# Performance work log

Hardware: AMD Instinct MI355X
Metric: run time of the kernel (lower is better)

The kernel has to match this reference:

```python
import jax, jax.numpy as jnp
import numpy as np

GRID_SIZE = 5
SPLINE_ORDER = 3
GRID_LO, GRID_HI = -3.0, 3.0
B, IN_DIM, UNITS, SUB_DIM, NSUB = 4096, 512, 1024, 512, 3


def make_grid(in_features):
    h = (GRID_HI - GRID_LO) / GRID_SIZE
    g = jnp.arange(-SPLINE_ORDER, GRID_SIZE + SPLINE_ORDER + 1, dtype=jnp.float32) * h + GRID_LO
    return jnp.broadcast_to(g, (in_features, g.shape[0]))  # (in, 12)


def b_splines(x, grid):
    # x: (..., in), grid: (in, G) -> (..., in, grid_size + spline_order)
    x = x[..., None]
    bases = ((x >= grid[:, :-1]) & (x < grid[:, 1:])).astype(x.dtype)
    for k in range(1, SPLINE_ORDER + 1):
        left = (x - grid[:, :-(k + 1)]) / (grid[:, k:-1] - grid[:, :-(k + 1)])
        right = (grid[:, k + 1:] - x) / (grid[:, k + 1:] - grid[:, 1:-k])
        bases = left * bases[..., :-1] + right * bases[..., 1:]
    return bases


def setup_inputs() -> dict:
    key = jax.random.key(0)
    ks = jax.random.split(key, 16)
    sw = lambda k, shape, scale: jax.random.normal(k, shape, dtype=jnp.float32) * scale
    inp = {
        'x': sw(ks[0], (B, IN_DIM), 1.0),
        'h0': sw(ks[1], (B, UNITS), 0.1),
        'c0': sw(ks[2], (B, UNITS), 0.1),
        'sub_states': sw(ks[3], (NSUB, B, SUB_DIM), 0.1),
        'kernel': sw(ks[4], (IN_DIM, UNITS * 3), 1.0 / np.sqrt(IN_DIM)),
        'recurrent_kernel': sw(ks[5], (UNITS, UNITS * 3), 1.0 / np.sqrt(UNITS)),
        'bias': jnp.zeros((UNITS * 3,), jnp.float32).at[UNITS:2 * UNITS].set(1.0),
        'sub_kernel_inputs': sw(ks[6], (NSUB, IN_DIM, SUB_DIM), 1.0 / np.sqrt(IN_DIM)),
        'sub_kernel_states': sw(ks[7], (NSUB, SUB_DIM, SUB_DIM), 1.0 / np.sqrt(SUB_DIM)),
        'sub_recurrent_kernel': sw(ks[8], (NSUB, SUB_DIM * 2), 0.5),
        'base_weight': sw(ks[9], (NSUB, SUB_DIM, SUB_DIM), 1.0 / np.sqrt(SUB_DIM)),
        'spline_weight': sw(ks[10], (NSUB, SUB_DIM, SUB_DIM, GRID_SIZE + SPLINE_ORDER), 0.02),
        'spline_scaler': sw(ks[11], (NSUB, SUB_DIM, SUB_DIM), 1.0),
        'aggregated_weight': sw(ks[12], (NSUB * SUB_DIM, UNITS), 1.0 / np.sqrt(NSUB * SUB_DIM)),
        'aggregated_bias': jnp.zeros((UNITS,), jnp.float32),
    }
    return inp


def reference(x, h0, c0, sub_states, kernel, recurrent_kernel, bias,
              sub_kernel_inputs, sub_kernel_states, sub_recurrent_kernel,
              base_weight, spline_weight, spline_scaler,
              aggregated_weight, aggregated_bias):
    grid = make_grid(SUB_DIM)

    # LSTM-style gates: gates = sigmoid(x@W + h@U + b)
    z = x @ kernel + h0 @ recurrent_kernel + bias
    g = jax.nn.sigmoid(z)
    i, f, c_gate = jnp.split(g, 3, axis=-1)
    c_new = f * c0 + i * jnp.tanh(c_gate)

    # Sub-layer inputs: agg[k] = x @ Wx[k] + sub_state[k] @ Wh[k]  -> (k, b, sub_in)
    agg = (jnp.einsum('bi,kis->kbs', x, sub_kernel_inputs)
           + jnp.einsum('kbo,kos->kbs', sub_states, sub_kernel_states))

    # KANLinear: base branch + spline branch (stacked over k sub-layers)
    base_out = jnp.einsum('kbs,kos->kbo', jax.nn.silu(agg), base_weight)
    bases = b_splines(agg, grid)                         # (k, b, sub_in, 8)
    scaled_sw = spline_weight * spline_scaler[..., None]  # (k, out, in, 8)
    spline_out = jnp.einsum('kbic,koic->kbo', bases, scaled_sw)
    sub_out = base_out + spline_out                       # (k, b, sub_out)

    # Recurrent sub-state update
    rk_h = sub_recurrent_kernel[:, None, :SUB_DIM]
    rk_x = sub_recurrent_kernel[:, None, SUB_DIM:]
    new_sub_states = rk_h * sub_out + rk_x * sub_states

    # Output gate from aggregated sub-layer outputs
    agg_flat = jnp.transpose(sub_out, (1, 0, 2)).reshape(x.shape[0], NSUB * SUB_DIM)
    o = jax.nn.sigmoid(agg_flat @ aggregated_weight + aggregated_bias)
    h_new = o * jnp.tanh(c_new)
    return h_new, c_new, new_sub_states
```

## Files before the change

### kernel.cpp

```cpp
#include <hip/hip_runtime.h>

#define B_DIM   4096
#define INF     512
#define UNITS_  1024
#define SUBD    512
#define NSUB_   3
#define NBAS    8
#define G3K     (SUBD * NBAS)

typedef __attribute__((ext_vector_type(8))) short bf16x8_t;
typedef __attribute__((ext_vector_type(4))) float f32x4_t;
typedef unsigned short u16;

__device__ __forceinline__ u16 f2bf(float f) {
    union { float f; unsigned int u; } v; v.f = f;
    unsigned int r = v.u + 0x7fffu + ((v.u >> 16) & 1u);
    return (u16)(r >> 16);
}
__device__ __forceinline__ float bf2f(u16 h) {
    union { unsigned int u; float f; } v; v.u = ((unsigned int)h) << 16;
    return v.f;
}
__device__ __forceinline__ float sigm(float x) { return 1.0f / (1.0f + __expf(-x)); }
__device__ __forceinline__ float tanh_(float x) {
    float e = __expf(2.0f * x);
    return 1.0f - 2.0f / (e + 1.0f);
}

__device__ __forceinline__ void gload_lds16(const void* g, void* l) {
    __builtin_amdgcn_global_load_lds(
        (const __attribute__((address_space(1))) unsigned int*)g,
        (__attribute__((address_space(3))) unsigned int*)l, 16, 0, 0);
}

__global__ void k_f32_to_bf16(const float* __restrict__ in, u16* __restrict__ out, int n4) {
    int i = blockIdx.x * blockDim.x + threadIdx.x;
    if (i >= n4) return;
    float4 v = ((const float4*)in)[i];
    ushort4 r; r.x = f2bf(v.x); r.y = f2bf(v.y); r.z = f2bf(v.z); r.w = f2bf(v.w);
    ((ushort4*)out)[i] = r;
}

__global__ void k_ssw(const float* __restrict__ sw, const float* __restrict__ sc,
                      u16* __restrict__ out, int n4) {
    int i = blockIdx.x * blockDim.x + threadIdx.x;
    if (i >= n4) return;
    float4 v = ((const float4*)sw)[i];
    float s = sc[i >> 1];
    ushort4 r; r.x = f2bf(v.x * s); r.y = f2bf(v.y * s); r.z = f2bf(v.z * s); r.w = f2bf(v.w * s);
    ((ushort4*)out)[i] = r;
}

__global__ void k_tconv(const float* __restrict__ in, u16* __restrict__ out,
                        int R, int C, size_t inStride, size_t outStride) {
    in  += (size_t)blockIdx.z * inStride;
    out += (size_t)blockIdx.z * outStride;
    __shared__ float tile[32][33];
    int c0 = blockIdx.x * 32, r0 = blockIdx.y * 32;
    int tx = threadIdx.x, ty = threadIdx.y;
#pragma unroll
    for (int j = 0; j < 4; ++j)
        tile[ty + j * 8][tx] = in[(size_t)(r0 + ty + j * 8) * C + c0 + tx];
    __syncthreads();
#pragma unroll
    for (int j = 0; j < 4; ++j)
        out[(size_t)(c0 + ty + j * 8) * R + r0 + tx] = f2bf(tile[tx][ty + j * 8]);
}

__global__ void k_cnew(const u16* __restrict__ gbuf, const float* __restrict__ c0,
                       float* __restrict__ c_out, int n4) {
    int i = blockIdx.x * blockDim.x + threadIdx.x;
    if (i >= n4) return;
    int u4 = i * 4;
    int b = u4 >> 10, u = u4 & 1023;
    const u16* gr = gbuf + (size_t)b * 3072 + u;
    ushort4 gi = *(const ushort4*)gr;
    ushort4 gf = *(const ushort4*)(gr + 1024);
    ushort4 gc = *(const ushort4*)(gr + 2048);
    float4 c0v = ((const float4*)c0)[i];
    float4 r;
    r.x = bf2f(gf.x) * c0v.x + bf2f(gi.x) * tanh_(bf2f(gc.x));
    r.y = bf2f(gf.y) * c0v.y + bf2f(gi.y) * tanh_(bf2f(gc.y));
    r.z = bf2f(gf.z) * c0v.z + bf2f(gi.z) * tanh_(bf2f(gc.z));
    r.w = bf2f(gf.w) * c0v.w + bf2f(gi.w) * tanh_(bf2f(gc.w));
    ((float4*)c_out)[i] = r;
}

__global__ void k_bases(const float* __restrict__ agg, u16* __restrict__ bases,
                        u16* __restrict__ silu, int n) {
    for (int i = blockIdx.x * blockDim.x + threadIdx.x; i < n; i += gridDim.x * blockDim.x) {
        float x = agg[i];
        silu[i] = f2bf(x * sigm(x));
        float b[11];
#pragma unroll
        for (int j = 0; j < 11; ++j) {
            float tj  = 1.2f * (float)(j - 3) - 3.0f;
            float tj1 = 1.2f * (float)(j - 2) - 3.0f;
            b[j] = (x >= tj && x < tj1) ? 1.0f : 0.0f;
        }
#pragma unroll
        for (int k = 1; k <= 3; ++k) {
            float inv = 1.0f / (1.2f * (float)k);
#pragma unroll
            for (int j = 0; j < 11; ++j) {
                if (j > 10 - k) break;
                float tj   = 1.2f * (float)(j - 3) - 3.0f;
                float tjk1 = 1.2f * (float)(j + k - 2) - 3.0f;
                b[j] = (x - tj) * inv * b[j] + (tjk1 - x) * inv * b[j + 1];
            }
        }
        bf16x8_t v;
#pragma unroll
        for (int j = 0; j < 8; ++j) v[j] = (short)f2bf(b[j]);
        *(bf16x8_t*)(bases + (size_t)i * 8) = v;
    }
}

struct Seg { const u16* A; const u16* B; int ldA; int ldB; int nkt; };

template<int NS, int BN>
__device__ __forceinline__ void gemm_core(const Seg (&segs)[NS], int rowBase, int colBase,
                                          u16* ldsA, u16* ldsB, f32x4_t (&acc)[4][BN / 32]) {
    constexpr int NACC = BN / 32;
    constexpr int NBC  = BN / 8;
    constexpr int PER  = (16 + NBC) / 4;
    const int t = threadIdx.x;
    const int lane = t & 63, wave = t >> 6;
    const int wR = (wave >> 1) * 64, wC = (wave & 1) * (BN / 2);
    const int l15 = lane & 15, lk = (lane >> 4) * 8;
    const int sr = lane >> 3;
    const int scol = (lane & 7) * 8;
#pragma unroll
    for (int s = 0; s < NS; ++s) {
        const u16* Ag = segs[s].A + (size_t)rowBase * segs[s].ldA;
        const u16* Bg = segs[s].B + (size_t)colBase * segs[s].ldB;
        const int ldA = segs[s].ldA, ldB = segs[s].ldB, nkt = segs[s].nkt;
        for (int kt = 0; kt < nkt; ++kt) {
            __syncthreads();
#pragma unroll
            for (int i = 0; i < PER; ++i) {
                int ci = wave * PER + i;
                if (ci < 16) {
                    int r = ci * 8 + sr;
                    gload_lds16(Ag + (size_t)r * ldA + kt * 64 + scol, ldsA + ci * 512);
                } else {
                    int cb = ci - 16;
                    int r = cb * 8 + sr;
                    gload_lds16(Bg + (size_t)r * ldB + kt * 64 + scol, ldsB + cb * 512);
                }
            }
            __syncthreads();
#pragma unroll
            for (int kk = 0; kk < 2; ++kk) {
                bf16x8_t a[4], b[NACC];
#pragma unroll
                for (int m = 0; m < 4; ++m)
                    a[m] = *(const bf16x8_t*)(ldsA + (wR + m * 16 + l15) * 64 + kk * 32 + lk);
#pragma unroll
                for (int n = 0; n < NACC; ++n)
                    b[n] = *(const bf16x8_t*)(ldsB + (wC + n * 16 + l15) * 64 + kk * 32 + lk);
#pragma unroll
                for (int m = 0; m < 4; ++m)
#pragma unroll
                    for (int n = 0; n < NACC; ++n)
                        acc[m][n] = __builtin_amdgcn_mfma_f32_16x16x32_bf16(a[m], b[n], acc[m][n], 0, 0, 0);
            }
        }
    }
}

template<int NCOL, int NROW, int NWG, bool SWZ>
__device__ __forceinline__ void decode_wg(int o, int& col, int& row, int& kz) {
    int wg = o;
    if (SWZ) {
        constexpr int q = NWG / 8, r = NWG % 8;
        int xcd = o & 7, idx = o >> 3;
        wg = (xcd < r ? xcd * (q + 1) : r * (q + 1) + (xcd - r) * q) + idx;
    }
    col = wg % NCOL; int tmp = wg / NCOL; row = tmp % NROW; kz = tmp / NROW;
}

#define GEMM_PRE(BN, NCOL, NROW, NWG, SWZ)                                 \
    __shared__ u16 ldsA[128 * 64];                                         \
    __shared__ u16 ldsB[BN * 64];                                          \
    int col_, row_, kz_;                                                   \
    decode_wg<NCOL, NROW, NWG, SWZ>(blockIdx.x, col_, row_, kz_);          \
    int rowBase = row_ * 128, colBase = col_ * BN;                         \
    f32x4_t acc[4][BN / 32];                                               \
    _Pragma("unroll") for (int m = 0; m < 4; ++m)                          \
        _Pragma("unroll") for (int n = 0; n < BN / 32; ++n)                \
            acc[m][n] = (f32x4_t){0.f, 0.f, 0.f, 0.f};

#define EPI_IDX(BN)                                                        \
    const int lane = threadIdx.x & 63, wave = threadIdx.x >> 6;            \
    const int wR = (wave >> 1) * 64, wC = (wave & 1) * (BN / 2);           \
    const int l15 = lane & 15, r4 = (lane >> 4) * 4;

__global__ __launch_bounds__(256) void k_gemm1(const u16* xb, const u16* h0b,
                                               const u16* kT, const u16* rkT,
                                               const float* __restrict__ bias,
                                               u16* __restrict__ gbuf) {
    GEMM_PRE(128, 24, 32, 768, false);
    Seg segs[2] = { { xb, kT, INF, INF, INF / 64 },
                    { h0b, rkT, UNITS_, UNITS_, UNITS_ / 64 } };
    gemm_core<2, 128>(segs, rowBase, colBase, ldsA, ldsB, acc);
    EPI_IDX(128);
#pragma unroll
    for (int m = 0; m < 4; ++m)
#pragma unroll
        for (int n = 0; n < 4; ++n)
#pragma unroll
            for (int j = 0; j < 4; ++j) {
                int row = rowBase + wR + m * 16 + r4 + j;
                int col = colBase + wC + n * 16 + l15;
                gbuf[(size_t)row * 3072 + col] = f2bf(sigm(acc[m][n][j] + bias[col]));
            }
}

__global__ __launch_bounds__(256) void k_gemm2(const u16* xb, const u16* ssb,
                                               const u16* skiT, const u16* sksT,
                                               float* __restrict__ agg) {
    GEMM_PRE(64, 8, 32, 768, false);
    int k = kz_;
    Seg segs[2] = { { xb, skiT + (size_t)k * SUBD * INF, INF, INF, INF / 64 },
                    { ssb + (size_t)k * B_DIM * SUBD, sksT + (size_t)k * SUBD * SUBD, SUBD, SUBD, SUBD / 64 } };
    gemm_core<2, 64>(segs, rowBase, colBase, ldsA, ldsB, acc);
    EPI_IDX(64);
#pragma unroll
    for (int m = 0; m < 4; ++m)
#pragma unroll
        for (int n = 0; n < 2; ++n)
#pragma unroll
            for (int j = 0; j < 4; ++j) {
                int row = rowBase + wR + m * 16 + r4 + j;
                int col = colBase + wC + n * 16 + l15;
                agg[((size_t)k * B_DIM + row) * SUBD + col] = acc[m][n][j];
            }
}

__global__ __launch_bounds__(256) void k_gemm3(const u16* silu, const u16* bases,
                                               const u16* bwb, const u16* sswb,
                                               const float* __restrict__ srk,
                                               const float* __restrict__ ss,
                                               float* __restrict__ nss_out,
                                               u16* __restrict__ subfl) {
    GEMM_PRE(64, 8, 32, 768, true);
    int k = kz_;
    Seg segs[2] = { { silu + (size_t)k * B_DIM * SUBD, bwb + (size_t)k * SUBD * SUBD, SUBD, SUBD, SUBD / 64 },
                    { bases + (size_t)k * B_DIM * G3K, sswb + (size_t)k * SUBD * G3K, G3K, G3K, G3K / 64 } };
    gemm_core<2, 64>(segs, rowBase, colBase, ldsA, ldsB, acc);
    EPI_IDX(64);
#pragma unroll
    for (int m = 0; m < 4; ++m)
#pragma unroll
        for (int n = 0; n < 2; ++n)
#pragma unroll
            for (int j = 0; j < 4; ++j) {
                int row = rowBase + wR + m * 16 + r4 + j;
                int col = colBase + wC + n * 16 + l15;
                float so = acc[m][n][j];
                float rh = srk[k * 1024 + col];
                float rx = srk[k * 1024 + 512 + col];
                size_t o = ((size_t)k * B_DIM + row) * SUBD + col;
                nss_out[o] = rh * so + rx * ss[o];
                subfl[(size_t)row * 1536 + k * SUBD + col] = f2bf(so);
            }
}

__global__ __launch_bounds__(256) void k_gemm4(const u16* subfl, const u16* awT,
                                               const float* __restrict__ abias,
                                               const float* __restrict__ c_new,
                                               float* __restrict__ h_out) {
    GEMM_PRE(64, 16, 32, 512, false);
    Seg segs[1] = { { subfl, awT, 1536, 1536, 1536 / 64 } };
    gemm_core<1, 64>(segs, rowBase, colBase, ldsA, ldsB, acc);
    EPI_IDX(64);
#pragma unroll
    for (int m = 0; m < 4; ++m)
#pragma unroll
        for (int n = 0; n < 2; ++n)
#pragma unroll
            for (int j = 0; j < 4; ++j) {
                int row = rowBase + wR + m * 16 + r4 + j;
                int col = colBase + wC + n * 16 + l15;
                float ov = sigm(acc[m][n][j] + abias[col]);
                h_out[(size_t)row * 1024 + col] = ov * tanh_(c_new[(size_t)row * 1024 + col]);
            }
}

extern "C" void kernel_launch(void* const* d_in, const int* in_sizes, int n_in,
                              void* d_out, int out_size, void* d_ws, size_t ws_size,
                              hipStream_t stream) {
    const float* x    = (const float*)d_in[0];
    const float* h0   = (const float*)d_in[1];
    const float* c0   = (const float*)d_in[2];
    const float* ss   = (const float*)d_in[3];
    const float* Wk   = (const float*)d_in[4];
    const float* Wr   = (const float*)d_in[5];
    const float* bias = (const float*)d_in[6];
    const float* ski  = (const float*)d_in[7];
    const float* sks  = (const float*)d_in[8];
    const float* srk  = (const float*)d_in[9];
    const float* bw   = (const float*)d_in[10];
    const float* sw   = (const float*)d_in[11];
    const float* sc   = (const float*)d_in[12];
    const float* aw   = (const float*)d_in[13];
    const float* ab   = (const float*)d_in[14];

    float* out_h   = (float*)d_out;
    float* out_c   = out_h + (size_t)B_DIM * UNITS_;
    float* out_nss = out_c + (size_t)B_DIM * UNITS_;

    char* w = (char*)d_ws;
    auto take = [&](size_t bytes) -> char* {
        char* p = w; w += (bytes + 255) & ~(size_t)255; return p;
    };
    u16*   xb    = (u16*)take((size_t)B_DIM * INF * 2);
    u16*   h0b   = (u16*)take((size_t)B_DIM * UNITS_ * 2);
    u16*   ssb   = (u16*)take((size_t)NSUB_ * B_DIM * SUBD * 2);
    u16*   kT    = (u16*)take((size_t)3072 * INF * 2);
    u16*   rkT   = (u16*)take((size_t)3072 * UNITS_ * 2);
    u16*   skiT  = (u16*)take((size_t)NSUB_ * SUBD * INF * 2);
    u16*   sksT  = (u16*)take((size_t)NSUB_ * SUBD * SUBD * 2);
    u16*   bwb   = (u16*)take((size_t)NSUB_ * SUBD * SUBD * 2);
    u16*   sswb  = (u16*)take((size_t)NSUB_ * SUBD * G3K * 2);
    u16*   awT   = (u16*)take((size_t)UNITS_ * 1536 * 2);
    float* agg   = (float*)take((size_t)NSUB_ * B_DIM * SUBD * 4);
    u16*   siluB = (u16*)take((size_t)NSUB_ * B_DIM * SUBD * 2);
    u16*   subfl = (u16*)take((size_t)B_DIM * 1536 * 2);
    u16*   basesB= (u16*)take((size_t)NSUB_ * B_DIM * G3K * 2);
    u16*   gbuf  = basesB;

    dim3 tb(256);
    k_f32_to_bf16<<<(B_DIM * INF / 4 + 255) / 256, tb, 0, stream>>>(x, xb, B_DIM * INF / 4);
    k_f32_to_bf16<<<(B_DIM * UNITS_ / 4 + 255) / 256, tb, 0, stream>>>(h0, h0b, B_DIM * UNITS_ / 4);
    k_f32_to_bf16<<<(NSUB_ * B_DIM * SUBD / 4 + 255) / 256, tb, 0, stream>>>(ss, ssb, NSUB_ * B_DIM * SUBD / 4);
    k_f32_to_bf16<<<(NSUB_ * SUBD * SUBD / 4 + 255) / 256, tb, 0, stream>>>(bw, bwb, NSUB_ * SUBD * SUBD / 4);
    k_ssw<<<(NSUB_ * SUBD * G3K / 4 + 255) / 256, tb, 0, stream>>>(sw, sc, sswb, NSUB_ * SUBD * G3K / 4);
    dim3 tt(32, 8);
    k_tconv<<<dim3(3072 / 32, INF / 32, 1), tt, 0, stream>>>(Wk, kT, INF, 3072, 0, 0);
    k_tconv<<<dim3(3072 / 32, UNITS_ / 32, 1), tt, 0, stream>>>(Wr, rkT, UNITS_, 3072, 0, 0);
    k_tconv<<<dim3(SUBD / 32, INF / 32, NSUB_), tt, 0, stream>>>(ski, skiT, INF, SUBD,
                                                                 (size_t)INF * SUBD, (size_t)SUBD * INF);
    k_tconv<<<dim3(SUBD / 32, SUBD / 32, NSUB_), tt, 0, stream>>>(sks, sksT, SUBD, SUBD,
                                                                  (size_t)SUBD * SUBD, (size_t)SUBD * SUBD);
    k_tconv<<<dim3(UNITS_ / 32, 1536 / 32, 1), tt, 0, stream>>>(aw, awT, 1536, UNITS_, 0, 0);

    k_gemm1<<<768, tb, 0, stream>>>(xb, h0b, kT, rkT, bias, gbuf);
    k_gemm2<<<768, tb, 0, stream>>>(xb, ssb, skiT, sksT, agg);
    k_cnew<<<(B_DIM * UNITS_ / 4 + 255) / 256, tb, 0, stream>>>(gbuf, c0, out_c, B_DIM * UNITS_ / 4);

    k_bases<<<4096, tb, 0, stream>>>(agg, basesB, siluB, NSUB_ * B_DIM * SUBD);

    k_gemm3<<<768, tb, 0, stream>>>(siluB, basesB, bwb, sswb, srk, ss, out_nss, subfl);
    k_gemm4<<<512, tb, 0, stream>>>(subfl, awT, ab, out_c, out_h);
}
```

Measured before the change: 500.9 us.

## Double-buffer LDS in shared GEMM core and shrink gemm1 tile width

```diff
diff --git a/kernel.cpp b/kernel.cpp
--- a/kernel.cpp
+++ b/kernel.cpp
@@ -120,52 +120,73 @@
 
 template<int NS, int BN>
 __device__ __forceinline__ void gemm_core(const Seg (&segs)[NS], int rowBase, int colBase,
-                                          u16* ldsA, u16* ldsB, f32x4_t (&acc)[4][BN / 32]) {
+                                          u16* lds, f32x4_t (&acc)[4][BN / 32]) {
     constexpr int NACC = BN / 32;
     constexpr int NBC  = BN / 8;
     constexpr int PER  = (16 + NBC) / 4;
+    constexpr int AELE = 128 * 64;
+    constexpr int BELE = BN * 64;
+    constexpr int BUF  = AELE + BELE;
     const int t = threadIdx.x;
     const int lane = t & 63, wave = t >> 6;
     const int wR = (wave >> 1) * 64, wC = (wave & 1) * (BN / 2);
     const int l15 = lane & 15, lk = (lane >> 4) * 8;
     const int sr = lane >> 3;
     const int scol = (lane & 7) * 8;
-#pragma unroll
-    for (int s = 0; s < NS; ++s) {
-        const u16* Ag = segs[s].A + (size_t)rowBase * segs[s].ldA;
-        const u16* Bg = segs[s].B + (size_t)colBase * segs[s].ldB;
-        const int ldA = segs[s].ldA, ldB = segs[s].ldB, nkt = segs[s].nkt;
-        for (int kt = 0; kt < nkt; ++kt) {
-            __syncthreads();
-#pragma unroll
-            for (int i = 0; i < PER; ++i) {
-                int ci = wave * PER + i;
-                if (ci < 16) {
-                    int r = ci * 8 + sr;
-                    gload_lds16(Ag + (size_t)r * ldA + kt * 64 + scol, ldsA + ci * 512);
-                } else {
-                    int cb = ci - 16;
-                    int r = cb * 8 + sr;
-                    gload_lds16(Bg + (size_t)r * ldB + kt * 64 + scol, ldsB + cb * 512);
-                }
-            }
-            __syncthreads();
-#pragma unroll
-            for (int kk = 0; kk < 2; ++kk) {
-                bf16x8_t a[4], b[NACC];
-#pragma unroll
-                for (int m = 0; m < 4; ++m)
-                    a[m] = *(const bf16x8_t*)(ldsA + (wR + m * 16 + l15) * 64 + kk * 32 + lk);
+
+    int NT = 0;
+#pragma unroll
+    for (int s = 0; s < NS; ++s) NT += segs[s].nkt;
+
+    auto stage = [&](int kt, int buf) {
+        const u16* Ag; const u16* Bg; int ldA, ldB, kl = kt;
+        if (NS == 1 || kt < segs[0].nkt) {
+            Ag = segs[0].A; Bg = segs[0].B; ldA = segs[0].ldA; ldB = segs[0].ldB;
+        } else {
+            Ag = segs[NS - 1].A; Bg = segs[NS - 1].B;
+            ldA = segs[NS - 1].ldA; ldB = segs[NS - 1].ldB;
+            kl = kt - segs[0].nkt;
+        }
+        const u16* As = Ag + (size_t)rowBase * ldA + kl * 64 + scol;
+        const u16* Bs = Bg + (size_t)colBase * ldB + kl * 64 + scol;
+        u16* dA = lds + buf * BUF;
+        u16* dB = dA + AELE;
+#pragma unroll
+        for (int i = 0; i < PER; ++i) {
+            int ci = wave * PER + i;
+            if (ci < 16) {
+                gload_lds16(As + (size_t)(ci * 8 + sr) * ldA, dA + ci * 512);
+            } else {
+                int cb = ci - 16;
+                gload_lds16(Bs + (size_t)(cb * 8 + sr) * ldB, dB + cb * 512);
+            }
+        }
+    };
+
+    stage(0, 0);
+    __syncthreads();
+    int cur = 0;
+    for (int kt = 0; kt < NT; ++kt) {
+        if (kt + 1 < NT) stage(kt + 1, cur ^ 1);
+        const u16* lA = lds + cur * BUF;
+        const u16* lB = lA + AELE;
+#pragma unroll
+        for (int kk = 0; kk < 2; ++kk) {
+            bf16x8_t a[4], b[NACC];
+#pragma unroll
+            for (int m = 0; m < 4; ++m)
+                a[m] = *(const bf16x8_t*)(lA + (wR + m * 16 + l15) * 64 + kk * 32 + lk);
+#pragma unroll
+            for (int n = 0; n < NACC; ++n)
+                b[n] = *(const bf16x8_t*)(lB + (wC + n * 16 + l15) * 64 + kk * 32 + lk);
+#pragma unroll
+            for (int m = 0; m < 4; ++m)
 #pragma unroll
                 for (int n = 0; n < NACC; ++n)
-                    b[n] = *(const bf16x8_t*)(ldsB + (wC + n * 16 + l15) * 64 + kk * 32 + lk);
-#pragma unroll
-                for (int m = 0; m < 4; ++m)
-#pragma unroll
-                    for (int n = 0; n < NACC; ++n)
-                        acc[m][n] = __builtin_amdgcn_mfma_f32_16x16x32_bf16(a[m], b[n], acc[m][n], 0, 0, 0);
-            }
-        }
+                    acc[m][n] = __builtin_amdgcn_mfma_f32_16x16x32_bf16(a[m], b[n], acc[m][n], 0, 0, 0);
+        }
+        __syncthreads();
+        cur ^= 1;
     }
 }
 
@@ -181,8 +202,7 @@
 }
 
 #define GEMM_PRE(BN, NCOL, NROW, NWG, SWZ)                                 \
-    __shared__ u16 ldsA[128 * 64];                                         \
-    __shared__ u16 ldsB[BN * 64];                                          \
+    __shared__ u16 lds[2 * (128 * 64 + BN * 64)];                          \
     int col_, row_, kz_;                                                   \
     decode_wg<NCOL, NROW, NWG, SWZ>(blockIdx.x, col_, row_, kz_);          \
     int rowBase = row_ * 128, colBase = col_ * BN;                         \
@@ -200,15 +220,15 @@
                                                const u16* kT, const u16* rkT,
                                                const float* __restrict__ bias,
                                                u16* __restrict__ gbuf) {
-    GEMM_PRE(128, 24, 32, 768, false);
+    GEMM_PRE(64, 48, 32, 1536, false);
     Seg segs[2] = { { xb, kT, INF, INF, INF / 64 },
                     { h0b, rkT, UNITS_, UNITS_, UNITS_ / 64 } };
-    gemm_core<2, 128>(segs, rowBase, colBase, ldsA, ldsB, acc);
-    EPI_IDX(128);
+    gemm_core<2, 64>(segs, rowBase, colBase, lds, acc);
+    EPI_IDX(64);
 #pragma unroll
     for (int m = 0; m < 4; ++m)
 #pragma unroll
-        for (int n = 0; n < 4; ++n)
+        for (int n = 0; n < 2; ++n)
 #pragma unroll
             for (int j = 0; j < 4; ++j) {
                 int row = rowBase + wR + m * 16 + r4 + j;
@@ -224,7 +244,7 @@
     int k = kz_;
     Seg segs[2] = { { xb, skiT + (size_t)k * SUBD * INF, INF, INF, INF / 64 },
                     { ssb + (size_t)k * B_DIM * SUBD, sksT + (size_t)k * SUBD * SUBD, SUBD, SUBD, SUBD / 64 } };
-    gemm_core<2, 64>(segs, rowBase, colBase, ldsA, ldsB, acc);
+    gemm_core<2, 64>(segs, rowBase, colBase, lds, acc);
     EPI_IDX(64);
 #pragma unroll
     for (int m = 0; m < 4; ++m)
@@ -248,7 +268,7 @@
     int k = kz_;
     Seg segs[2] = { { silu + (size_t)k * B_DIM * SUBD, bwb + (size_t)k * SUBD * SUBD, SUBD, SUBD, SUBD / 64 },
                     { bases + (size_t)k * B_DIM * G3K, sswb + (size_t)k * SUBD * G3K, G3K, G3K, G3K / 64 } };
-    gemm_core<2, 64>(segs, rowBase, colBase, ldsA, ldsB, acc);
+    gemm_core<2, 64>(segs, rowBase, colBase, lds, acc);
     EPI_IDX(64);
 #pragma unroll
     for (int m = 0; m < 4; ++m)
@@ -273,7 +293,7 @@
                                                float* __restrict__ h_out) {
     GEMM_PRE(64, 16, 32, 512, false);
     Seg segs[1] = { { subfl, awT, 1536, 1536, 1536 / 64 } };
-    gemm_core<1, 64>(segs, rowBase, colBase, ldsA, ldsB, acc);
+    gemm_core<1, 64>(segs, rowBase, colBase, lds, acc);
     EPI_IDX(64);
 #pragma unroll
     for (int m = 0; m < 4; ++m)
@@ -346,7 +366,7 @@
                                                                   (size_t)SUBD * SUBD, (size_t)SUBD * SUBD);
     k_tconv<<<dim3(UNITS_ / 32, 1536 / 32, 1), tt, 0, stream>>>(aw, awT, 1536, UNITS_, 0, 0);
 
-    k_gemm1<<<768, tb, 0, stream>>>(xb, h0b, kT, rkT, bias, gbuf);
+    k_gemm1<<<1536, tb, 0, stream>>>(xb, h0b, kT, rkT, bias, gbuf);
     k_gemm2<<<768, tb, 0, stream>>>(xb, ssb, skiT, sksT, agg);
     k_cnew<<<(B_DIM * UNITS_ / 4 + 255) / 256, tb, 0, stream>>>(gbuf, c0, out_c, B_DIM * UNITS_ / 4);
 
```

Result: faster. 471.8 us (-5.8%).
